# Optimization experiments

Measured on AMD Instinct MI355X. Metric: run time of the kernel, lower is better.

Reference implementation:

```python
import jax, jax.numpy as jnp
import numpy as np

VOCAB = 12149
EMB = 50
TAGS = 9
HID = 128
START = 7
B, T = 256, 512


def setup_inputs() -> dict:
    key = jax.random.key(0)
    ks = jax.random.split(key, 12)
    s = 0.05
    return {
        "inputs": jax.random.randint(ks[0], (B, T), 0, VOCAB),
        "seq_label": jax.random.randint(ks[1], (B, T), 0, TAGS),
        "emb": jax.random.normal(ks[2], (VOCAB, EMB), jnp.float32) * s,
        "enc_Wx": jax.random.normal(ks[3], (EMB, HID), jnp.float32) * s,
        "enc_Wh": jax.random.normal(ks[4], (HID, HID), jnp.float32) * s,
        "enc_b": jnp.zeros((HID,), jnp.float32),
        "dec_emb": jax.random.normal(ks[5], (TAGS, EMB), jnp.float32) * s,
        "dec_Wx": jax.random.normal(ks[6], (EMB, HID), jnp.float32) * s,
        "dec_Wh": jax.random.normal(ks[7], (HID, HID), jnp.float32) * s,
        "dec_b": jnp.zeros((HID,), jnp.float32),
        "W": jax.random.normal(ks[8], (HID, TAGS), jnp.float32) * s,
        "b": jnp.zeros((TAGS,), jnp.float32),
    }


def _rnn(x_tbd, h0, Wx, Wh, b, collect):
    # x_tbd: [T, B, E]; SimpleRNN cell: h_t = tanh(x_t Wx + h_{t-1} Wh + b)
    def step(h, xt):
        h = jnp.tanh(xt @ Wx + h @ Wh + b)
        return h, (h if collect else None)
    hT, hs = jax.lax.scan(step, h0, x_tbd)
    return hT, hs


def reference(inputs, seq_label, emb, enc_Wx, enc_Wh, enc_b,
              dec_emb, dec_Wx, dec_Wh, dec_b, W, b):
    Bsz = inputs.shape[0]
    h0 = jnp.zeros((Bsz, HID), jnp.float32)
    # Encoder: only the final state is used as the decoder's initial state
    x = emb[inputs]                                  # [B, T, EMB]
    state, _ = _rnn(jnp.swapaxes(x, 0, 1), h0, enc_Wx, enc_Wh, enc_b, False)
    # Teacher forcing: prepend START token, drop last label
    dec_in = jnp.concatenate(
        [jnp.full((Bsz, 1), START, seq_label.dtype), seq_label], axis=1)[:, :-1]
    dx = dec_emb[dec_in]                             # [B, T, EMB]
    _, hs = _rnn(jnp.swapaxes(dx, 0, 1), state, dec_Wx, dec_Wh, dec_b, True)
    hs = jnp.swapaxes(hs, 0, 1)                      # [B, T, HID]
    return hs @ W + b                                # [B, T, TAGS]
```

## Files before the change

### kernel.cpp

```cpp
#include <hip/hip_runtime.h>
#include <hip/hip_bf16.h>

#define VOCAB 12149
#define EMB 50
#define TAGS 9
#define HID 128
#define START_TOK 7
#define BSZ 256
#define TLEN 512

__device__ __forceinline__ float tanh_fast(float x) {
  float e = __expf(2.0f * x);
  return 1.0f - 2.0f * __builtin_amdgcn_rcpf(e + 1.0f);
}

template<int CTRL>
__device__ __forceinline__ float dpp_mov(float x) {
  return __int_as_float(__builtin_amdgcn_update_dpp(
      0, __float_as_int(x), CTRL, 0xF, 0xF, true));
}
#define DPP_XOR1 0xB1
#define DPP_XOR2 0x4E
#define DPP_HALF_MIRROR 0x141
#define DPP_MIRROR 0x140

__global__ __launch_bounds__(128) void exw_kernel(
    const float* __restrict__ emb, const float* __restrict__ Wx,
    const float* __restrict__ bv, float* __restrict__ exw)
{
  __shared__ float wx_s[EMB * HID];
  __shared__ float emb_s[8 * EMB];
  const int tid = threadIdx.x;
  const int v0 = blockIdx.x * 8;
  for (int idx = tid; idx < EMB * HID; idx += 128) wx_s[idx] = Wx[idx];
  for (int idx = tid; idx < 8 * EMB; idx += 128) {
    int r = idx / EMB;
    int e = idx - r * EMB;
    int v = v0 + r;
    emb_s[idx] = (v < VOCAB) ? emb[v * EMB + e] : 0.0f;
  }
  __syncthreads();
  const float bj = bv[tid];
  for (int r = 0; r < 8; ++r) {
    int v = v0 + r;
    if (v >= VOCAB) break;
    float acc = bj;
#pragma unroll
    for (int e = 0; e < EMB; ++e) acc += emb_s[r * EMB + e] * wx_s[e * HID + tid];
    exw[v * HID + tid] = acc;
  }
}

__global__ __launch_bounds__(256) void rnn_kernel(
    const int* __restrict__ inputs, const int* __restrict__ labels,
    const float* __restrict__ exw,
    const float* __restrict__ encWh,
    const float* __restrict__ dembG, const float* __restrict__ decWx,
    const float* __restrict__ decWh, const float* __restrict__ decb,
    const float* __restrict__ W, const float* __restrict__ bout,
    float* __restrict__ out)
{
  __shared__ float h_s[2][HID];
  __shared__ int tok_s[TLEN];
  __shared__ int lab_s[TLEN];
  __shared__ float dxw_s[TAGS * HID];
  __shared__ float demb_s[TAGS * EMB];

  const int i = threadIdx.x;
  const int w = i >> 6;
  const int lane = i & 63;
  const int q = lane & 3;
  const int jj = lane >> 2;
  const int jbase = w * 32 + jj * 2;
  const int jout = jbase + (q & 1);
  const int bidx = blockIdx.x;

  tok_s[i] = inputs[bidx * TLEN + i];
  tok_s[i + 256] = inputs[bidx * TLEN + 256 + i];
  lab_s[i] = labels[bidx * TLEN + i];
  lab_s[i + 256] = labels[bidx * TLEN + 256 + i];
  for (int idx = i; idx < TAGS * EMB; idx += 256) demb_s[idx] = dembG[idx];
  if (i < HID) h_s[0][i] = 0.0f;

  float2 wv[32];
#pragma unroll
  for (int r = 0; r < 8; ++r) {
    const int kb = q * 32 + ((r + 2 * q) & 7) * 4;
#pragma unroll
    for (int c = 0; c < 4; ++c)
      wv[r * 4 + c] = *(const float2*)(&encWh[(kb + c) * HID + jbase]);
  }

  const int oo = i >> 4;
  const int part = i & 15;
  const int s0 = (part >> 2) & 1;
  float wp[8];
  float bo = 0.0f;
#pragma unroll
  for (int u = 0; u < 8; ++u) wp[u] = 0.0f;
  if (oo < TAGS) {
#pragma unroll
    for (int s = 0; s < 2; ++s)
#pragma unroll
      for (int c = 0; c < 4; ++c)
        wp[s * 4 + c] = W[(part * 8 + (s ^ s0) * 4 + c) * TAGS + oo];
    bo = bout[oo];
  }
  __syncthreads();

  for (int task = i; task < TAGS * HID; task += 256) {
    int tag = task >> 7;
    int j2 = task & 127;
    float acc = decb[j2];
#pragma unroll
    for (int e = 0; e < EMB; ++e) acc += demb_s[tag * EMB + e] * decWx[e * HID + j2];
    dxw_s[task] = acc;
  }
  __syncthreads();

  const float* exw_j = exw + jout;
  const bool odd = (q & 1) != 0;
  int cur = 0;

  float xv0 = exw_j[tok_s[0] * HID];
  float xv1 = exw_j[tok_s[1] * HID];
  float xv2 = exw_j[tok_s[2] * HID];
  float xv3 = exw_j[tok_s[3] * HID];

#pragma unroll 4
  for (int t = 0; t < TLEN; ++t) {
    int tn = (t + 4 < TLEN) ? t + 4 : TLEN - 1;
    float xvn = exw_j[tok_s[tn] * HID];

    const float4* h4 = (const float4*)(h_s[cur]) + q * 8;
    float a0x = 0, a0y = 0, a1x = 0, a1y = 0;
#pragma unroll
    for (int r = 0; r < 8; ++r) {
      float4 hv = h4[(r + 2 * q) & 7];
      float2 w0 = wv[r * 4 + 0], w1 = wv[r * 4 + 1];
      float2 w2 = wv[r * 4 + 2], w3 = wv[r * 4 + 3];
      a0x += hv.x * w0.x; a0y += hv.y * w1.x; a0x += hv.z * w2.x; a0y += hv.w * w3.x;
      a1x += hv.x * w0.y; a1y += hv.y * w1.y; a1x += hv.z * w2.y; a1y += hv.w * w3.y;
    }
    float a0 = a0x + a0y, a1 = a1x + a1y;
    float keep = odd ? a1 : a0;
    float send = odd ? a0 : a1;
    float v = keep + dpp_mov<DPP_XOR1>(send);
    v += dpp_mov<DPP_XOR2>(v);
    float hnew = tanh_fast(v + xv0);
    h_s[cur ^ 1][jout] = hnew;
    __syncthreads();
    cur ^= 1;
    xv0 = xv1; xv1 = xv2; xv2 = xv3; xv3 = xvn;
  }

#pragma unroll
  for (int r = 0; r < 8; ++r) {
    const int kb = q * 32 + ((r + 2 * q) & 7) * 4;
#pragma unroll
    for (int c = 0; c < 4; ++c)
      wv[r * 4 + c] = *(const float2*)(&decWh[(kb + c) * HID + jbase]);
  }

#pragma unroll 2
  for (int t = 0; t < TLEN; ++t) {
    int lab = (t == 0) ? START_TOK : lab_s[t - 1];
    float xv = dxw_s[lab * HID + jout];

    const float4* h4 = (const float4*)(h_s[cur]) + q * 8;
    float a0x = 0, a0y = 0, a1x = 0, a1y = 0;
#pragma unroll
    for (int r = 0; r < 8; ++r) {
      float4 hv = h4[(r + 2 * q) & 7];
      float2 w0 = wv[r * 4 + 0], w1 = wv[r * 4 + 1];
      float2 w2 = wv[r * 4 + 2], w3 = wv[r * 4 + 3];
      a0x += hv.x * w0.x; a0y += hv.y * w1.x; a0x += hv.z * w2.x; a0y += hv.w * w3.x;
      a1x += hv.x * w0.y; a1y += hv.y * w1.y; a1x += hv.z * w2.y; a1y += hv.w * w3.y;
    }
    float a0 = a0x + a0y, a1 = a1x + a1y;
    float keep = odd ? a1 : a0;
    float send = odd ? a0 : a1;
    float v = keep + dpp_mov<DPP_XOR1>(send);
    v += dpp_mov<DPP_XOR2>(v);
    float hnew = tanh_fast(v + xv);
    h_s[cur ^ 1][jout] = hnew;
    __syncthreads();
    cur ^= 1;

    if (oo < TAGS) {
      const float4* hp = (const float4*)(h_s[cur]) + part * 2;
      float pacc = 0.0f;
#pragma unroll
      for (int s = 0; s < 2; ++s) {
        float4 u = hp[s ^ s0];
        pacc += u.x * wp[s * 4 + 0]; pacc += u.y * wp[s * 4 + 1];
        pacc += u.z * wp[s * 4 + 2]; pacc += u.w * wp[s * 4 + 3];
      }
      pacc += dpp_mov<DPP_XOR1>(pacc);
      pacc += dpp_mov<DPP_XOR2>(pacc);
      pacc += dpp_mov<DPP_HALF_MIRROR>(pacc);
      pacc += dpp_mov<DPP_MIRROR>(pacc);
      if (part == 0) out[(bidx * TLEN + t) * TAGS + oo] = pacc + bo;
    }
  }
}

extern "C" void kernel_launch(void* const* d_in, const int* in_sizes, int n_in,
                              void* d_out, int out_size, void* d_ws, size_t ws_size,
                              hipStream_t stream) {
  const int* inputs   = (const int*)d_in[0];
  const int* labels   = (const int*)d_in[1];
  const float* emb    = (const float*)d_in[2];
  const float* encWx  = (const float*)d_in[3];
  const float* encWh  = (const float*)d_in[4];
  const float* encb   = (const float*)d_in[5];
  const float* demb   = (const float*)d_in[6];
  const float* decWx  = (const float*)d_in[7];
  const float* decWh  = (const float*)d_in[8];
  const float* decb   = (const float*)d_in[9];
  const float* W      = (const float*)d_in[10];
  const float* bo     = (const float*)d_in[11];
  float* out = (float*)d_out;

  float* exw = (float*)d_ws;

  exw_kernel<<<(VOCAB + 7) / 8, 128, 0, stream>>>(emb, encWx, encb, exw);
  rnn_kernel<<<BSZ, 256, 0, stream>>>(inputs, labels, exw, encWh,
                                      demb, decWx, decWh, decb, W, bo, out);
}
```

Measured before the change: 360.4 us.

## Remap RNN recurrence to 16-lane groups with packed v2f FMAs

Reorganizes the per-step h·Wh matvec so each 16-lane group owns 8 hidden outputs. Each lane handles 8 k-values and 4 output pairs using packed two-wide FMAs (v_pk_fma). The partial sums are combined with a DPP tree (xor1, xor2, row-rotate 4, row-rotate 8), and lanes 0-3 each write two outputs. The intent is to halve the FMA instruction count in the serial recurrence and vectorize the h and x loads. The cost is a deeper cross-lane reduction, redundant tanh in 12 of every 16 lanes, and reliance on DPP row-rotate semantics to be correct.

```diff
diff --git a/kernel.cpp b/kernel.cpp
--- a/kernel.cpp
+++ b/kernel.cpp
@@ -9,6 +9,8 @@
 #define BSZ 256
 #define TLEN 512
 
+typedef float v2f __attribute__((ext_vector_type(2)));
+
 __device__ __forceinline__ float tanh_fast(float x) {
   float e = __expf(2.0f * x);
   return 1.0f - 2.0f * __builtin_amdgcn_rcpf(e + 1.0f);
@@ -19,8 +21,17 @@
   return __int_as_float(__builtin_amdgcn_update_dpp(
       0, __float_as_int(x), CTRL, 0xF, 0xF, true));
 }
+template<int CTRL>
+__device__ __forceinline__ v2f dpp2(v2f x) {
+  v2f r;
+  r.x = dpp_mov<CTRL>(x.x);
+  r.y = dpp_mov<CTRL>(x.y);
+  return r;
+}
 #define DPP_XOR1 0xB1
 #define DPP_XOR2 0x4E
+#define DPP_ROR4 0x124
+#define DPP_ROR8 0x128
 #define DPP_HALF_MIRROR 0x141
 #define DPP_MIRROR 0x140
 
@@ -51,6 +62,26 @@
   }
 }
 
+__device__ __forceinline__ void dot_step(const float4 hA, const float4 hB,
+                                         const v2f* __restrict__ wv, v2f acc[4]) {
+  const float ha[4] = {hA.x, hA.y, hA.z, hA.w};
+  const float hb[4] = {hB.x, hB.y, hB.z, hB.w};
+#pragma unroll
+  for (int c = 0; c < 4; ++c) {
+    v2f h2 = {ha[c], ha[c]};
+#pragma unroll
+    for (int m = 0; m < 4; ++m)
+      acc[m] = __builtin_elementwise_fma(h2, wv[c * 4 + m], acc[m]);
+  }
+#pragma unroll
+  for (int c = 0; c < 4; ++c) {
+    v2f h2 = {hb[c], hb[c]};
+#pragma unroll
+    for (int m = 0; m < 4; ++m)
+      acc[m] = __builtin_elementwise_fma(h2, wv[16 + c * 4 + m], acc[m]);
+  }
+}
+
 __global__ __launch_bounds__(256) void rnn_kernel(
     const int* __restrict__ inputs, const int* __restrict__ labels,
     const float* __restrict__ exw,
@@ -60,19 +91,19 @@
     const float* __restrict__ W, const float* __restrict__ bout,
     float* __restrict__ out)
 {
-  __shared__ float h_s[2][HID];
+  __shared__ __align__(16) float h_s[2][HID];
+  __shared__ __align__(16) float dxw_s[TAGS * HID];
   __shared__ int tok_s[TLEN];
   __shared__ int lab_s[TLEN];
-  __shared__ float dxw_s[TAGS * HID];
   __shared__ float demb_s[TAGS * EMB];
 
   const int i = threadIdx.x;
   const int w = i >> 6;
   const int lane = i & 63;
-  const int q = lane & 3;
-  const int jj = lane >> 2;
-  const int jbase = w * 32 + jj * 2;
-  const int jout = jbase + (q & 1);
+  const int l = lane & 15;
+  const int g = lane >> 4;
+  const int q = l & 3;
+  const int jb = w * 32 + g * 8;
   const int bidx = blockIdx.x;
 
   tok_s[i] = inputs[bidx * TLEN + i];
@@ -82,14 +113,15 @@
   for (int idx = i; idx < TAGS * EMB; idx += 256) demb_s[idx] = dembG[idx];
   if (i < HID) h_s[0][i] = 0.0f;
 
-  float2 wv[32];
-#pragma unroll
-  for (int r = 0; r < 8; ++r) {
-    const int kb = q * 32 + ((r + 2 * q) & 7) * 4;
+  v2f wv[32];
+#pragma unroll
+  for (int s = 0; s < 2; ++s)
 #pragma unroll
     for (int c = 0; c < 4; ++c)
-      wv[r * 4 + c] = *(const float2*)(&encWh[(kb + c) * HID + jbase]);
-  }
+#pragma unroll
+      for (int m = 0; m < 4; ++m)
+        wv[s * 16 + c * 4 + m] =
+            *(const v2f*)&encWh[(s * 64 + 4 * l + c) * HID + jb + 2 * (m ^ q)];
 
   const int oo = i >> 4;
   const int part = i & 15;
@@ -118,72 +150,70 @@
   }
   __syncthreads();
 
-  const float* exw_j = exw + jout;
-  const bool odd = (q & 1) != 0;
+  const float* exw_q = exw + jb + 2 * q;
   int cur = 0;
 
-  float xv0 = exw_j[tok_s[0] * HID];
-  float xv1 = exw_j[tok_s[1] * HID];
-  float xv2 = exw_j[tok_s[2] * HID];
-  float xv3 = exw_j[tok_s[3] * HID];
+  v2f xv0 = *(const v2f*)&exw_q[tok_s[0] * HID];
+  v2f xv1 = *(const v2f*)&exw_q[tok_s[1] * HID];
+  v2f xv2 = *(const v2f*)&exw_q[tok_s[2] * HID];
+  v2f xv3 = *(const v2f*)&exw_q[tok_s[3] * HID];
 
 #pragma unroll 4
   for (int t = 0; t < TLEN; ++t) {
     int tn = (t + 4 < TLEN) ? t + 4 : TLEN - 1;
-    float xvn = exw_j[tok_s[tn] * HID];
-
-    const float4* h4 = (const float4*)(h_s[cur]) + q * 8;
-    float a0x = 0, a0y = 0, a1x = 0, a1y = 0;
-#pragma unroll
-    for (int r = 0; r < 8; ++r) {
-      float4 hv = h4[(r + 2 * q) & 7];
-      float2 w0 = wv[r * 4 + 0], w1 = wv[r * 4 + 1];
-      float2 w2 = wv[r * 4 + 2], w3 = wv[r * 4 + 3];
-      a0x += hv.x * w0.x; a0y += hv.y * w1.x; a0x += hv.z * w2.x; a0y += hv.w * w3.x;
-      a1x += hv.x * w0.y; a1y += hv.y * w1.y; a1x += hv.z * w2.y; a1y += hv.w * w3.y;
-    }
-    float a0 = a0x + a0y, a1 = a1x + a1y;
-    float keep = odd ? a1 : a0;
-    float send = odd ? a0 : a1;
-    float v = keep + dpp_mov<DPP_XOR1>(send);
-    v += dpp_mov<DPP_XOR2>(v);
-    float hnew = tanh_fast(v + xv0);
-    h_s[cur ^ 1][jout] = hnew;
+    v2f xvn = *(const v2f*)&exw_q[tok_s[tn] * HID];
+
+    float4 hA = *(const float4*)&h_s[cur][4 * l];
+    float4 hB = *(const float4*)&h_s[cur][64 + 4 * l];
+    v2f acc[4] = {v2f{0.f, 0.f}, v2f{0.f, 0.f}, v2f{0.f, 0.f}, v2f{0.f, 0.f}};
+    dot_step(hA, hB, wv, acc);
+
+    acc[0] += dpp2<DPP_XOR1>(acc[1]);
+    acc[2] += dpp2<DPP_XOR1>(acc[3]);
+    acc[0] += dpp2<DPP_XOR2>(acc[2]);
+    acc[0] += dpp2<DPP_ROR4>(acc[0]);
+    acc[0] += dpp2<DPP_ROR8>(acc[0]);
+
+    v2f u = acc[0] + xv0;
+    v2f hn;
+    hn.x = tanh_fast(u.x);
+    hn.y = tanh_fast(u.y);
+    if (l < 4) *(v2f*)&h_s[cur ^ 1][jb + 2 * q] = hn;
     __syncthreads();
     cur ^= 1;
     xv0 = xv1; xv1 = xv2; xv2 = xv3; xv3 = xvn;
   }
 
 #pragma unroll
-  for (int r = 0; r < 8; ++r) {
-    const int kb = q * 32 + ((r + 2 * q) & 7) * 4;
+  for (int s = 0; s < 2; ++s)
 #pragma unroll
     for (int c = 0; c < 4; ++c)
-      wv[r * 4 + c] = *(const float2*)(&decWh[(kb + c) * HID + jbase]);
-  }
+#pragma unroll
+      for (int m = 0; m < 4; ++m)
+        wv[s * 16 + c * 4 + m] =
+            *(const v2f*)&decWh[(s * 64 + 4 * l + c) * HID + jb + 2 * (m ^ q)];
 
 #pragma unroll 2
   for (int t = 0; t < TLEN; ++t) {
     int lab = (t == 0) ? START_TOK : lab_s[t - 1];
-    float xv = dxw_s[lab * HID + jout];
-
-    const float4* h4 = (const float4*)(h_s[cur]) + q * 8;
-    float a0x = 0, a0y = 0, a1x = 0, a1y = 0;
-#pragma unroll
-    for (int r = 0; r < 8; ++r) {
-      float4 hv = h4[(r + 2 * q) & 7];
-      float2 w0 = wv[r * 4 + 0], w1 = wv[r * 4 + 1];
-      float2 w2 = wv[r * 4 + 2], w3 = wv[r * 4 + 3];
-      a0x += hv.x * w0.x; a0y += hv.y * w1.x; a0x += hv.z * w2.x; a0y += hv.w * w3.x;
-      a1x += hv.x * w0.y; a1y += hv.y * w1.y; a1x += hv.z * w2.y; a1y += hv.w * w3.y;
-    }
-    float a0 = a0x + a0y, a1 = a1x + a1y;
-    float keep = odd ? a1 : a0;
-    float send = odd ? a0 : a1;
-    float v = keep + dpp_mov<DPP_XOR1>(send);
-    v += dpp_mov<DPP_XOR2>(v);
-    float hnew = tanh_fast(v + xv);
-    h_s[cur ^ 1][jout] = hnew;
+    v2f xv = *(const v2f*)&dxw_s[lab * HID + jb + 2 * q];
+
+    float4 hA = *(const float4*)&h_s[cur][4 * l];
+    float4 hB = *(const float4*)&h_s[cur][64 + 4 * l];
+    v2f acc[4] = {v2f{0.f, 0.f}, v2f{0.f, 0.f}, v2f{0.f, 0.f}, v2f{0.f, 0.f}};
+    dot_step(hA, hB, wv, acc);
+
+    acc[0] += dpp2<DPP_XOR1>(acc[1]);
+    acc[2] += dpp2<DPP_XOR1>(acc[3]);
+    acc[0] += dpp2<DPP_XOR2>(acc[2]);
+    acc[0] += dpp2<DPP_ROR4>(acc[0]);
+    acc[0] += dpp2<DPP_ROR8>(acc[0]);
+
+    v2f u = acc[0] + xv;
+    v2f hn;
+    hn.x = tanh_fast(u.x);
+    hn.y = tanh_fast(u.y);
+    if (l < 4) *(v2f*)&h_s[cur ^ 1][jb + 2 * q] = hn;
     __syncthreads();
     cur ^= 1;
 
@@ -192,9 +222,9 @@
       float pacc = 0.0f;
 #pragma unroll
       for (int s = 0; s < 2; ++s) {
-        float4 u = hp[s ^ s0];
-        pacc += u.x * wp[s * 4 + 0]; pacc += u.y * wp[s * 4 + 1];
-        pacc += u.z * wp[s * 4 + 2]; pacc += u.w * wp[s * 4 + 3];
+        float4 uu = hp[s ^ s0];
+        pacc += uu.x * wp[s * 4 + 0]; pacc += uu.y * wp[s * 4 + 1];
+        pacc += uu.z * wp[s * 4 + 2]; pacc += uu.w * wp[s * 4 + 3];
       }
       pacc += dpp_mov<DPP_XOR1>(pacc);
       pacc += dpp_mov<DPP_XOR2>(pacc);
```

Result: slower. 400.5 us (+11.1%).
